# Kernel optimization log

Hardware: AMD Instinct MI355X
Metric: run time of the kernel (lower is better)

Reference implementation:

```python
import jax, jax.numpy as jnp
import numpy as np

KS = 3          # kernel_size
C_IN = 64       # channel_size
F_OUT = 128     # filters
K_CONNECT = 4   # n_connect (<= KS*KS)
N_POS = KS * KS


def setup_inputs() -> dict:
    key = jax.random.key(0)
    k1, k2, k3, k4 = jax.random.split(key, 4)
    x = jax.random.normal(k1, (16, 128, 128, C_IN), dtype=jnp.float32)
    kern = jax.random.normal(k2, (KS, KS, C_IN, F_OUT), dtype=jnp.float32) * 0.1  # he_uniform-ish
    b = jnp.zeros((F_OUT,), dtype=jnp.float32)
    D = jax.random.normal(k3, (KS, KS, C_IN, F_OUT), dtype=jnp.float32) * 0.5     # trainable logits
    gumbel_u = jax.random.uniform(k4, (1, F_OUT, C_IN, N_POS), dtype=jnp.float32)  # BS=1 uniform noise
    return {"x": x, "kern": kern, "b": b, "D": D, "gumbel_u": gumbel_u}


def dps_topk(D, u, k, temp):
    # D: [KS, KS, C, F]; raw reshape to [F, C, KS*KS] exactly as the TF code does
    F_, C_ = D.shape[3], D.shape[2]
    N_ = D.shape[0] * D.shape[0]
    logits = D.reshape(F_, C_, N_)                       # [F, C, N]
    gn = -0.001 * jnp.log(-jnp.log(u + 1e-20) + 1e-20)   # [1, F, C, N] scaled Gumbel noise
    pert = logits[None] + gn                             # [1, F, C, N]
    # top-k by value (descending), then top-k of the indices -> indices sorted descending
    _, idx = jax.lax.top_k(pert, k)                      # [1, F, C, k] int32
    idx_desc, _ = jax.lax.top_k(idx, k)                  # sorted descending
    topk = idx_desc[..., ::-1]                           # ascending indices
    hard = jax.nn.one_hot(topk, N_, dtype=logits.dtype)  # [1, F, C, k, N]
    cum = jnp.cumsum(hard, axis=-2) - hard               # exclusive cumsum over k (hard is 0/1)
    prob_exp = jnp.exp(logits)[None, :, :, None, :]      # [1, F, C, 1, N] broadcast over k
    soft = jax.nn.softmax(
        (jnp.log(prob_exp * (1.0 - cum + 1e-20)) + gn[:, :, :, None, :]) / temp,
        axis=-1,
    )
    # straight-through: hard forward, soft backward
    return jax.lax.stop_gradient(hard - soft) + soft


def reference(x, kern, b, D, gumbel_u):
    temp = 1.0  # step=0 -> epoch=0 -> initial temperature
    A_ = dps_topk(D, gumbel_u, K_CONNECT, temp)          # [1, F, C, k, N]
    A = A_[0].sum(axis=-2).reshape(KS, KS, C_IN, F_OUT)  # raw reshape, as in the TF code
    # binarize kernel with straight-through estimator
    t1 = jnp.sign(kern)
    t2 = jnp.clip(0.4 * kern, -1.0, 1.0)                 # 2*hard_sigmoid(k) - 1
    ww = jax.lax.stop_gradient(t1 - t2) + t2
    AW = A * ww                                          # sparse-masked binary kernel
    y = jax.lax.conv_general_dilated(
        x, AW, window_strides=(1, 1), padding='SAME',
        dimension_numbers=('NHWC', 'HWIO', 'NHWC'),
    )
    y = y + b
    return jax.nn.relu(y)
```

## Files before the change

kernel.cpp:

```cpp
#include <hip/hip_runtime.h>
#include <hip/hip_bf16.h>
#include <math.h>

#define KS 3
#define C_IN 64
#define F_OUT 128
#define NPOS 9
#define HH 128
#define WWID 128
#define NB 16

typedef __attribute__((ext_vector_type(8))) short bf16x8;
typedef __attribute__((ext_vector_type(4))) float f32x4;

__device__ __forceinline__ unsigned short f2bf(float f) {
  union { float f; unsigned u; } v; v.f = f;
  unsigned u = v.u;
  return (unsigned short)((u + 0x7FFFu + ((u >> 16) & 1u)) >> 16);
}
__device__ __forceinline__ unsigned cvtpk(float lo, float hi) {
  unsigned r;
  asm("v_cvt_pk_bf16_f32 %0, %1, %2" : "=v"(r) : "v"(lo), "v"(hi));
  return r;
}
__device__ __forceinline__ bf16x8 pack8(float4 v0, float4 v1) {
  union { unsigned u[4]; bf16x8 v; } r;
  r.u[0] = cvtpk(v0.x, v0.y); r.u[1] = cvtpk(v0.z, v0.w);
  r.u[2] = cvtpk(v1.x, v1.y); r.u[3] = cvtpk(v1.z, v1.w);
  return r.v;
}
__device__ __forceinline__ void gload16(const void* g, void* l) {
  __builtin_amdgcn_global_load_lds(
      (const __attribute__((address_space(1))) unsigned int*)g,
      (__attribute__((address_space(3))) unsigned int*)l, 16, 0, 0);
}

__global__ void compute_aw(const float* __restrict__ kern,
                           const float* __restrict__ D,
                           const float* __restrict__ gu,
                           unsigned short* __restrict__ AWsw) {
  int t = blockIdx.x * blockDim.x + threadIdx.x;
  if (t >= F_OUT * C_IN) return;
  int base = t * NPOS;
  float pert[NPOS];
#pragma unroll
  for (int n = 0; n < NPOS; ++n) {
    float u = gu[base + n];
    float g = -0.001f * logf(-logf(u + 1e-20f) + 1e-20f);
    pert[n] = D[base + n] + g;
  }
  unsigned mask = 0;
#pragma unroll
  for (int k = 0; k < 4; ++k) {
    int best = 0; float bv = -INFINITY;
#pragma unroll
    for (int n = 0; n < NPOS; ++n) {
      bool taken = (mask >> n) & 1;
      if (!taken && pert[n] > bv) { bv = pert[n]; best = n; }
    }
    mask |= (1u << best);
  }
#pragma unroll
  for (int n = 0; n < NPOS; ++n) {
    int L = base + n;
    float kv = kern[L];
    float sg = (kv > 0.f) ? 1.f : ((kv < 0.f) ? -1.f : 0.f);
    float v = ((mask >> n) & 1) ? sg : 0.f;
    int f = L & (F_OUT - 1);
    int r = L >> 7;
    int c = r & (C_IN - 1);
    int p = r >> 6;
    int s = p / 3, pl = p % 3;
    int g = c >> 3;
    int slot = g ^ (f & 7);
    int off = s * 24576 + ((pl * F_OUT + f) * 8 + slot) * 8 + (c & 7);
    AWsw[off] = f2bf(v);
  }
}

__global__ __launch_bounds__(512, 2)
void conv5(const float* __restrict__ x,
           const unsigned short* __restrict__ AWsw,
           const float* __restrict__ bias,
           float* __restrict__ out) {
  __shared__ __align__(16) unsigned short As[6 * 130 * 64];
  __shared__ __align__(16) unsigned short Bs[3 * F_OUT * 64];

  int tid = threadIdx.x;
  int lane = tid & 63, wave = tid >> 6;
  int lr = lane & 15, lg = lane >> 4;

  int bid = blockIdx.x;
  int wg = (bid & 7) * 64 + (bid >> 3);
  int n = wg >> 5;
  int h0 = (wg & 31) * 4;

  int ro = wave >> 1;
  int m0 = (wave & 1) * 64;

  bf16x8 z = {};
  if (h0 == 0 || h0 == 124) {
    for (int t = tid; t < 6240; t += 512)
      *reinterpret_cast<bf16x8*>(As + t * 8) = z;
  } else if (tid < 96) {
    int r = tid >> 4, k = tid & 15;
    int pp = (k >> 3) ? 129 : 0, c8 = k & 7;
    *reinterpret_cast<bf16x8*>((char*)As + r * 16640 + pp * 128 +
                               ((c8 ^ (pp & 7)) << 4)) = z;
  }
  __syncthreads();

#pragma unroll
  for (int k = 0; k < 6; ++k) {
    int wi = wave * 6 + k;
    gload16(AWsw + wi * 512 + lane * 8, (char*)Bs + wi * 1024);
  }

  const float* xim = x + ((long long)n * HH) * WWID * C_IN;
#pragma unroll
  for (int t = 0; t < 12; ++t) {
    int cid = t * 512 + tid;
    int r = cid >> 10, rem = cid & 1023;
    int px = rem >> 3, c8 = rem & 7;
    int hh = h0 - 1 + r;
    if ((unsigned)hh < (unsigned)HH) {
      const float* sp = xim + (long long)hh * (WWID * C_IN) + px * C_IN + c8 * 8;
      float4 v0 = *reinterpret_cast<const float4*>(sp);
      float4 v1 = *reinterpret_cast<const float4*>(sp + 4);
      int pp = px + 1;
      *reinterpret_cast<bf16x8*>((char*)As + r * 16640 + pp * 128 +
                                 ((c8 ^ (pp & 7)) << 4)) = pack8(v0, v1);
    }
  }
  __syncthreads();

  f32x4 acc[4][8] = {};
  bf16x8 pre[6];

#define PREFETCH(SN)                                                         \
  _Pragma("unroll")                                                          \
  for (int k = 0; k < 6; ++k)                                                \
    pre[k] = *reinterpret_cast<const bf16x8*>(                               \
        AWsw + (SN) * 24576 + (k * 512 + tid) * 8);

#define BWRITE()                                                             \
  _Pragma("unroll")                                                          \
  for (int k = 0; k < 6; ++k)                                                \
    *reinterpret_cast<bf16x8*>(Bs + (k * 512 + tid) * 8) = pre[k];

#define COMPUTE(S)                                                           \
  __builtin_amdgcn_s_setprio(1);                                             \
  _Pragma("unroll")                                                          \
  for (int pl = 0; pl < 3; ++pl) {                                           \
    _Pragma("unroll")                                                        \
    for (int ch = 0; ch < 2; ++ch) {                                         \
      bf16x8 b[8];                                                           \
      _Pragma("unroll")                                                      \
      for (int nf = 0; nf < 8; ++nf)                                         \
        b[nf] = *reinterpret_cast<const bf16x8*>(                            \
            (const char*)Bs + pl * 16384 + nf * 2048 + lr * 128 +            \
            (((ch * 4 + lg) ^ (lr & 7)) << 4));                              \
      bf16x8 a[4];                                                           \
      _Pragma("unroll")                                                      \
      for (int mfi = 0; mfi < 4; ++mfi) {                                    \
        int pxb = m0 + mfi * 16 + lr + pl;                                   \
        a[mfi] = *reinterpret_cast<const bf16x8*>(                           \
            (const char*)As + (ro + (S)) * 16640 + pxb * 128 +               \
            (((ch * 4 + lg) ^ (pxb & 7)) << 4));                             \
      }                                                                      \
      _Pragma("unroll")                                                      \
      for (int mfi = 0; mfi < 4; ++mfi)                                      \
        _Pragma("unroll")                                                    \
        for (int nf = 0; nf < 8; ++nf)                                       \
          acc[mfi][nf] = __builtin_amdgcn_mfma_f32_16x16x32_bf16(            \
              a[mfi], b[nf], acc[mfi][nf], 0, 0, 0);                         \
    }                                                                        \
  }                                                                          \
  __builtin_amdgcn_s_setprio(0);

  PREFETCH(1)
  COMPUTE(0)
  __syncthreads();
  BWRITE()
  __syncthreads();
  PREFETCH(2)
  COMPUTE(1)
  __syncthreads();
  BWRITE()
  __syncthreads();
  COMPUTE(2)

  float bi[8];
#pragma unroll
  for (int nf = 0; nf < 8; ++nf) bi[nf] = bias[nf * 16 + lr];
  int ho = h0 + ro;
  long long ob = ((long long)(n * HH + ho)) * WWID * F_OUT + lr;
#pragma unroll
  for (int mfi = 0; mfi < 4; ++mfi) {
#pragma unroll
    for (int r4 = 0; r4 < 4; ++r4) {
      int w = m0 + mfi * 16 + lg * 4 + r4;
      float* op = out + ob + (long long)w * F_OUT;
#pragma unroll
      for (int nf = 0; nf < 8; ++nf)
        op[nf * 16] = fmaxf(acc[mfi][nf][r4] + bi[nf], 0.f);
    }
  }
#undef PREFETCH
#undef BWRITE
#undef COMPUTE
}

extern "C" void kernel_launch(void* const* d_in, const int* in_sizes, int n_in,
                              void* d_out, int out_size, void* d_ws, size_t ws_size,
                              hipStream_t stream) {
  const float* x    = (const float*)d_in[0];
  const float* kern = (const float*)d_in[1];
  const float* bias = (const float*)d_in[2];
  const float* D    = (const float*)d_in[3];
  const float* gu   = (const float*)d_in[4];

  unsigned short* AWsw = (unsigned short*)d_ws;

  compute_aw<<<(F_OUT * C_IN + 255) / 256, 256, 0, stream>>>(kern, D, gu, AWsw);

  conv5<<<NB * (HH / 4), 512, 0, stream>>>(x, AWsw, bias, (float*)d_out);
}
```

Measured before the change: 59.46 us.

## Process eight output rows per block with a ring-buffered input tile and overlapped loads

Each block now computes two 4-row output tiles instead of one, keeping a 6-row LDS ring buffer of the input. The next input rows are issued into registers during compute and written to LDS between weight stages, so halo rows are reused and global loads overlap MFMA work. Boundary handling switches from branches to clamped loads with zero selects. The grid is halved, which lowers parallelism to 256 blocks and raises register pressure from the extra prefetch registers.

```diff
diff --git a/kernel.cpp b/kernel.cpp
--- a/kernel.cpp
+++ b/kernel.cpp
@@ -72,14 +72,13 @@
     int p = r >> 6;
     int s = p / 3, pl = p % 3;
     int g = c >> 3;
-    int slot = g ^ (f & 7);
-    int off = s * 24576 + ((pl * F_OUT + f) * 8 + slot) * 8 + (c & 7);
+    int off = s * 24576 + ((pl * F_OUT + f) * 8 + (g ^ (f & 7))) * 8 + (c & 7);
     AWsw[off] = f2bf(v);
   }
 }
 
 __global__ __launch_bounds__(512, 2)
-void conv5(const float* __restrict__ x,
+void conv7(const float* __restrict__ x,
            const unsigned short* __restrict__ AWsw,
            const float* __restrict__ bias,
            float* __restrict__ out) {
@@ -91,24 +90,22 @@
   int lr = lane & 15, lg = lane >> 4;
 
   int bid = blockIdx.x;
-  int wg = (bid & 7) * 64 + (bid >> 3);
-  int n = wg >> 5;
-  int h0 = (wg & 31) * 4;
+  int wg = (bid & 7) * 32 + (bid >> 3);
+  int n = wg >> 4;
+  int h0 = (wg & 15) * 8;
 
   int ro = wave >> 1;
   int m0 = (wave & 1) * 64;
 
+  const float* xim = x + ((long long)n * HH) * WWID * C_IN;
+
   bf16x8 z = {};
-  if (h0 == 0 || h0 == 124) {
-    for (int t = tid; t < 6240; t += 512)
-      *reinterpret_cast<bf16x8*>(As + t * 8) = z;
-  } else if (tid < 96) {
+  if (tid < 96) {
     int r = tid >> 4, k = tid & 15;
     int pp = (k >> 3) ? 129 : 0, c8 = k & 7;
     *reinterpret_cast<bf16x8*>((char*)As + r * 16640 + pp * 128 +
                                ((c8 ^ (pp & 7)) << 4)) = z;
   }
-  __syncthreads();
 
 #pragma unroll
   for (int k = 0; k < 6; ++k) {
@@ -116,26 +113,26 @@
     gload16(AWsw + wi * 512 + lane * 8, (char*)Bs + wi * 1024);
   }
 
-  const float* xim = x + ((long long)n * HH) * WWID * C_IN;
 #pragma unroll
   for (int t = 0; t < 12; ++t) {
     int cid = t * 512 + tid;
     int r = cid >> 10, rem = cid & 1023;
     int px = rem >> 3, c8 = rem & 7;
     int hh = h0 - 1 + r;
-    if ((unsigned)hh < (unsigned)HH) {
-      const float* sp = xim + (long long)hh * (WWID * C_IN) + px * C_IN + c8 * 8;
-      float4 v0 = *reinterpret_cast<const float4*>(sp);
-      float4 v1 = *reinterpret_cast<const float4*>(sp + 4);
-      int pp = px + 1;
-      *reinterpret_cast<bf16x8*>((char*)As + r * 16640 + pp * 128 +
-                                 ((c8 ^ (pp & 7)) << 4)) = pack8(v0, v1);
-    }
+    int hc = hh < 0 ? 0 : (hh > 127 ? 127 : hh);
+    const float* sp = xim + (long long)hc * (WWID * C_IN) + px * C_IN + c8 * 8;
+    float4 v0 = *reinterpret_cast<const float4*>(sp);
+    float4 v1 = *reinterpret_cast<const float4*>(sp + 4);
+    bf16x8 val = ((unsigned)hh < (unsigned)HH) ? pack8(v0, v1) : z;
+    int pp = px + 1;
+    *reinterpret_cast<bf16x8*>((char*)As + r * 16640 + pp * 128 +
+                               ((c8 ^ (pp & 7)) << 4)) = val;
   }
   __syncthreads();
 
   f32x4 acc[4][8] = {};
   bf16x8 pre[6];
+  float4 xv[8];
 
 #define PREFETCH(SN)                                                         \
   _Pragma("unroll")                                                          \
@@ -148,67 +145,133 @@
   for (int k = 0; k < 6; ++k)                                                \
     *reinterpret_cast<bf16x8*>(Bs + (k * 512 + tid) * 8) = pre[k];
 
-#define COMPUTE(S)                                                           \
-  __builtin_amdgcn_s_setprio(1);                                             \
-  _Pragma("unroll")                                                          \
-  for (int pl = 0; pl < 3; ++pl) {                                           \
+#define ISSUE_X(B)                                                           \
+  _Pragma("unroll")                                                          \
+  for (int c = 0; c < 4; ++c) {                                              \
+    int cid = c * 512 + tid;                                                 \
+    int rr = cid >> 10, rem = cid & 1023;                                    \
+    int px = rem >> 3, c8 = rem & 7;                                         \
+    int row = h0 + 5 + 2 * (B) + rr;                                         \
+    int hc = row > 127 ? 127 : row;                                          \
+    const float* sp = xim + (long long)hc * (WWID * C_IN) + px * C_IN + c8 * 8;\
+    xv[c * 2]     = *reinterpret_cast<const float4*>(sp);                    \
+    xv[c * 2 + 1] = *reinterpret_cast<const float4*>(sp + 4);                \
+  }
+
+#define DRAIN_X(B)                                                           \
+  _Pragma("unroll")                                                          \
+  for (int c = 0; c < 4; ++c) {                                              \
+    int cid = c * 512 + tid;                                                 \
+    int rr = cid >> 10, rem = cid & 1023;                                    \
+    int px = rem >> 3, c8 = rem & 7;                                         \
+    int row = h0 + 5 + 2 * (B) + rr;                                         \
+    bf16x8 val = (row < HH) ? pack8(xv[c * 2], xv[c * 2 + 1]) : z;           \
+    int sl = 2 * (B) + rr;                                                   \
+    int pp = px + 1;                                                         \
+    *reinterpret_cast<bf16x8*>((char*)As + sl * 16640 + pp * 128 +           \
+                               ((c8 ^ (pp & 7)) << 4)) = val;                \
+  }
+
+#define COMPUTE(T, S)                                                        \
+  {                                                                          \
+    int sl = ro + (S) + 4 * (T);                                             \
+    if (sl >= 6) sl -= 6;                                                    \
+    const char* arow = (const char*)As + sl * 16640;                         \
+    __builtin_amdgcn_s_setprio(1);                                           \
     _Pragma("unroll")                                                        \
     for (int ch = 0; ch < 2; ++ch) {                                         \
-      bf16x8 b[8];                                                           \
+      const int pl = (S);                                                    \
+      (void)pl;                                                              \
       _Pragma("unroll")                                                      \
-      for (int nf = 0; nf < 8; ++nf)                                         \
-        b[nf] = *reinterpret_cast<const bf16x8*>(                            \
-            (const char*)Bs + pl * 16384 + nf * 2048 + lr * 128 +            \
-            (((ch * 4 + lg) ^ (lr & 7)) << 4));                              \
-      bf16x8 a[4];                                                           \
+      for (int j = 0; j < 3; ++j) {                                          \
+        const char* bp = (const char*)Bs + j * 16384 + lr * 128 +            \
+                         (((ch * 4 + lg) ^ (lr & 7)) << 4);                  \
+        bf16x8 b[8];                                                         \
+        _Pragma("unroll")                                                    \
+        for (int nf = 0; nf < 8; ++nf)                                       \
+          b[nf] = *reinterpret_cast<const bf16x8*>(bp + nf * 2048);          \
+        bf16x8 a[4];                                                         \
+        _Pragma("unroll")                                                    \
+        for (int mfi = 0; mfi < 4; ++mfi) {                                  \
+          int pxb = m0 + mfi * 16 + lr + j;                                  \
+          a[mfi] = *reinterpret_cast<const bf16x8*>(                         \
+              arow + pxb * 128 + (((ch * 4 + lg) ^ (pxb & 7)) << 4));        \
+        }                                                                    \
+        _Pragma("unroll")                                                    \
+        for (int mfi = 0; mfi < 4; ++mfi)                                    \
+          _Pragma("unroll")                                                  \
+          for (int nf = 0; nf < 8; ++nf)                                     \
+            acc[mfi][nf] = __builtin_amdgcn_mfma_f32_16x16x32_bf16(          \
+                a[mfi], b[nf], acc[mfi][nf], 0, 0, 0);                       \
+      }                                                                      \
+    }                                                                        \
+    __builtin_amdgcn_s_setprio(0);                                           \
+  }
+
+#define EPILOGUE(T)                                                          \
+  {                                                                          \
+    float bi[8];                                                             \
+    _Pragma("unroll")                                                        \
+    for (int nf = 0; nf < 8; ++nf) bi[nf] = bias[nf * 16 + lr];              \
+    int ho = h0 + 4 * (T) + ro;                                              \
+    long long ob = ((long long)(n * HH + ho)) * WWID * F_OUT + lr;           \
+    _Pragma("unroll")                                                        \
+    for (int mfi = 0; mfi < 4; ++mfi) {                                      \
       _Pragma("unroll")                                                      \
-      for (int mfi = 0; mfi < 4; ++mfi) {                                    \
-        int pxb = m0 + mfi * 16 + lr + pl;                                   \
-        a[mfi] = *reinterpret_cast<const bf16x8*>(                           \
-            (const char*)As + (ro + (S)) * 16640 + pxb * 128 +               \
-            (((ch * 4 + lg) ^ (pxb & 7)) << 4));                             \
+      for (int r4 = 0; r4 < 4; ++r4) {                                       \
+        int w = m0 + mfi * 16 + lg * 4 + r4;                                 \
+        float* op = out + ob + (long long)w * F_OUT;                         \
+        _Pragma("unroll")                                                    \
+        for (int nf = 0; nf < 8; ++nf)                                       \
+          op[nf * 16] = fmaxf(acc[mfi][nf][r4] + bi[nf], 0.f);               \
       }                                                                      \
-      _Pragma("unroll")                                                      \
-      for (int mfi = 0; mfi < 4; ++mfi)                                      \
-        _Pragma("unroll")                                                    \
-        for (int nf = 0; nf < 8; ++nf)                                       \
-          acc[mfi][nf] = __builtin_amdgcn_mfma_f32_16x16x32_bf16(            \
-              a[mfi], b[nf], acc[mfi][nf], 0, 0, 0);                         \
     }                                                                        \
-  }                                                                          \
-  __builtin_amdgcn_s_setprio(0);
+  }
 
   PREFETCH(1)
-  COMPUTE(0)
-  __syncthreads();
-  BWRITE()
+  COMPUTE(0, 0)
+  __syncthreads();
+  BWRITE()
+  ISSUE_X(0)
   __syncthreads();
   PREFETCH(2)
-  COMPUTE(1)
-  __syncthreads();
-  BWRITE()
-  __syncthreads();
-  COMPUTE(2)
-
-  float bi[8];
-#pragma unroll
-  for (int nf = 0; nf < 8; ++nf) bi[nf] = bias[nf * 16 + lr];
-  int ho = h0 + ro;
-  long long ob = ((long long)(n * HH + ho)) * WWID * F_OUT + lr;
-#pragma unroll
-  for (int mfi = 0; mfi < 4; ++mfi) {
-#pragma unroll
-    for (int r4 = 0; r4 < 4; ++r4) {
-      int w = m0 + mfi * 16 + lg * 4 + r4;
-      float* op = out + ob + (long long)w * F_OUT;
-#pragma unroll
-      for (int nf = 0; nf < 8; ++nf)
-        op[nf * 16] = fmaxf(acc[mfi][nf][r4] + bi[nf], 0.f);
-    }
-  }
+  COMPUTE(0, 1)
+  __syncthreads();
+  BWRITE()
+  DRAIN_X(0)
+  ISSUE_X(1)
+  __syncthreads();
+  PREFETCH(0)
+  COMPUTE(0, 2)
+  __syncthreads();
+  BWRITE()
+  DRAIN_X(1)
+  __syncthreads();
+  PREFETCH(1)
+  EPILOGUE(0)
+#pragma unroll
+  for (int mfi = 0; mfi < 4; ++mfi)
+#pragma unroll
+    for (int nf = 0; nf < 8; ++nf) acc[mfi][nf] = (f32x4){0.f, 0.f, 0.f, 0.f};
+
+  COMPUTE(1, 0)
+  __syncthreads();
+  BWRITE()
+  __syncthreads();
+  PREFETCH(2)
+  COMPUTE(1, 1)
+  __syncthreads();
+  BWRITE()
+  __syncthreads();
+  COMPUTE(1, 2)
+  EPILOGUE(1)
+
 #undef PREFETCH
 #undef BWRITE
+#undef ISSUE_X
+#undef DRAIN_X
 #undef COMPUTE
+#undef EPILOGUE
 }
 
 extern "C" void kernel_launch(void* const* d_in, const int* in_sizes, int n_in,
@@ -224,5 +287,5 @@
 
   compute_aw<<<(F_OUT * C_IN + 255) / 256, 256, 0, stream>>>(kern, D, gu, AWsw);
 
-  conv5<<<NB * (HH / 4), 512, 0, stream>>>(x, AWsw, bias, (float*)d_out);
-}
+  conv7<<<NB * (HH / 8), 512, 0, stream>>>(x, AWsw, bias, (float*)d_out);
+}
```

New measurement: 64.56 us. +8.6%, slower.
